# Optimization experiments

Hardware: AMD Instinct MI355X
Metric: run time of the kernel (lower is better)

## Reference

```python
import jax, jax.numpy as jnp
import numpy as np


def setup_inputs() -> dict:
    key = jax.random.key(0)
    k1, k2, k3, k4 = jax.random.split(key, 4)
    B, V, P, C, R, N, OUT = 8, 4096, 32, 32, 2, 16, 32  # N=(l_max+1)^2, l_max=3
    signal = jax.random.normal(k1, (B, V, C), dtype=jnp.float32)
    patches_idx = jax.random.randint(k2, (B, V, P), 0, V, dtype=jnp.int32)
    conv_kernel = jax.random.normal(k3, (B, V, P, R, N), dtype=jnp.float32)
    kernel_weights = jax.random.normal(k4, (OUT, C, R, N), dtype=jnp.float32) * 0.05
    biases = jnp.zeros((OUT,), dtype=jnp.float32)
    return {
        "signal": signal,
        "patches_idx": patches_idx,
        "conv_kernel": conv_kernel,
        "kernel_weights": kernel_weights,
        "biases": biases,
    }


def reference(signal, patches_idx, conv_kernel, kernel_weights, biases):
    # Gather per-vertex tree-neighbor patches (tf.gather_nd with batch idx):
    # signal [B,V,C], patches_idx [B,V,P] -> patches [B,V,P,C]
    patches = jax.vmap(lambda s, i: s[i])(signal, patches_idx)
    # Bilinear contraction with precomputed SH conv kernel: [B,V,P,R,N] x [B,V,P,C]
    y = jnp.einsum('bvprn,bvpc->bvcrn', conv_kernel, patches)
    # Learned weights contraction: [OUT,C,R,N] x [B,V,C,R,N] -> [B,V,OUT]
    y = jnp.einsum('ijrn,bvjrn->bvi', kernel_weights, y)
    y = y + biases
    return jax.nn.relu(y)
```

## Files before the change

### kernel.cpp

```cpp
#include <hip/hip_runtime.h>


typedef __attribute__((ext_vector_type(8))) short bf16x8;
typedef __attribute__((ext_vector_type(4))) short short4v;
typedef __attribute__((ext_vector_type(16))) float f32x16;
typedef __attribute__((ext_vector_type(4))) float f32x4;

__device__ __forceinline__ unsigned short f2bf_rne(float f) {
    union { float f; unsigned int u; } x;
    x.f = f;
    unsigned int u = x.u;
    return (unsigned short)((u + 0x7fffu + ((u >> 16) & 1u)) >> 16);
}
__device__ __forceinline__ unsigned short f2bf_rh(float f) {
    union { float f; unsigned int u; } x;
    x.f = f;
    return (unsigned short)((x.u + 0x8000u) >> 16);
}

__global__ __launch_bounds__(256) void prep_kernel(
        const float* __restrict__ W, const float* __restrict__ sig,
        unsigned short* __restrict__ Wf, unsigned short* __restrict__ sigbf) {
    int tid = blockIdx.x * 256 + threadIdx.x;
    if (tid < 32768) {
        int j = tid & 7;
        int l = (tid >> 3) & 63;
        int pair = tid >> 9;
        int s = pair >> 1;
        int t = pair & 1;
        int i = 16 * t + (l & 15);
        int crn = 32 * s + 8 * (l >> 4) + j;
        Wf[tid] = f2bf_rne(W[i * 1024 + crn]);
    } else {
        int e = (tid - 32768) * 8;
        if (e < 8 * 4096 * 32) {
            f32x4 a = *(const f32x4*)(sig + e);
            f32x4 b = *(const f32x4*)(sig + e + 4);
            bf16x8 v;
            v[0] = (short)f2bf_rne(a[0]); v[1] = (short)f2bf_rne(a[1]);
            v[2] = (short)f2bf_rne(a[2]); v[3] = (short)f2bf_rne(a[3]);
            v[4] = (short)f2bf_rne(b[0]); v[5] = (short)f2bf_rne(b[1]);
            v[6] = (short)f2bf_rne(b[2]); v[7] = (short)f2bf_rne(b[3]);
            *(bf16x8*)(sigbf + e) = v;
        }
    }
}

__global__ __launch_bounds__(512, 8) void fused_kernel(
        const unsigned short* __restrict__ sigbf, const int* __restrict__ pidx,
        const float* __restrict__ ck, const unsigned short* __restrict__ Wf,
        const float* __restrict__ bias, float* __restrict__ out) {
    __shared__ __align__(16) unsigned short ckb[8 * 1024];
    __shared__ __align__(16) unsigned short T_lds[8 * 1032];
    const int tid = threadIdx.x;
    const int l = tid & 63;
    const int g = l >> 5;
    const int cc = l & 31;
    const int wu = __builtin_amdgcn_readfirstlane(tid >> 6);
    const int m0 = blockIdx.x * 8;
    const int b = m0 >> 12;
    const unsigned short* sgb = sigbf + (size_t)b * (4096 * 32);

    int rows[32];
    {
        const int* ip = pidx + (size_t)(m0 + wu) * 32;
        #pragma unroll
        for (int k = 0; k < 32; ++k) rows[k] = ip[k];
    }
    f32x4 st[4];
    {
        const f32x4* ckv = (const f32x4*)(ck + (size_t)(m0 + wu) * 1024);
        #pragma unroll
        for (int i = 0; i < 4; ++i) st[i] = ckv[i * 64 + l];
    }
    unsigned short ga[16];
    #pragma unroll
    for (int h = 0; h < 2; ++h) {
        #pragma unroll
        for (int j = 0; j < 8; ++j) {
            const int rlo = rows[h * 16 + j];
            const int rhi = rows[h * 16 + 8 + j];
            const int row = g ? rhi : rlo;
            ga[h * 8 + j] = sgb[row * 32 + cc];
        }
    }
    #pragma unroll
    for (int i = 0; i < 4; ++i) {
        union { f32x4 f; unsigned int u[4]; } x;
        x.f = st[i];
        short4v v = { (short)(x.u[0] >> 16), (short)(x.u[1] >> 16),
                      (short)(x.u[2] >> 16), (short)(x.u[3] >> 16) };
        *(short4v*)(ckb + wu * 1024 + (i * 64 + l) * 4) = v;
    }
    __syncthreads();

    {
        const unsigned short* ct = ckb + wu * 1024;
        f32x16 acc = {};
        #pragma unroll
        for (int h = 0; h < 2; ++h) {
            bf16x8 af, bfr;
            #pragma unroll
            for (int j = 0; j < 8; ++j) {
                const int p = h * 16 + 8 * g + j;
                af[j]  = (short)ga[h * 8 + j];
                bfr[j] = (short)ct[p * 32 + cc];
            }
            acc = __builtin_amdgcn_mfma_f32_32x32x16_bf16(af, bfr, acc, 0, 0, 0);
        }
        unsigned short* trow = T_lds + wu * 1032 + cc + g * 128;
        #pragma unroll
        for (int r = 0; r < 16; ++r)
            trow[((r & 3) + 8 * (r >> 2)) * 32] = f2bf_rh(acc[r]);
    }
    __syncthreads();

    f32x4 acc0 = {}, acc1 = {};
    const int lg = l >> 4;
    const int ln = l & 15;
    #pragma unroll
    for (int si = 0; si < 4; ++si) {
        const int s = 4 * wu + si;
        const bf16x8 af =
            *(const bf16x8*)(T_lds + (ln & 7) * 1032 + s * 32 + 8 * lg);
        const bf16x8* wrow = (const bf16x8*)(Wf + (size_t)(s * 2) * 512);
        const bf16x8 b0 = wrow[l];
        const bf16x8 b1 = wrow[64 + l];
        acc0 = __builtin_amdgcn_mfma_f32_16x16x32_bf16(af, b0, acc0, 0, 0, 0);
        acc1 = __builtin_amdgcn_mfma_f32_16x16x32_bf16(af, b1, acc1, 0, 0, 0);
    }
    __syncthreads();

    float* red = (float*)T_lds;
    {
        f32x4* rp = (f32x4*)(red + wu * 512);
        rp[l]      = acc0;
        rp[64 + l] = acc1;
    }
    __syncthreads();

    if (tid < 256) {
        const int bv  = tid >> 5;
        const int i   = tid & 31;
        const int t   = i >> 4;
        const int col = i & 15;
        const int lgi = bv >> 2;
        const int r   = bv & 3;
        const int li  = lgi * 16 + col;
        const int o   = t * 256 + li * 4 + r;
        float sum = 0.f;
        #pragma unroll
        for (int w2 = 0; w2 < 8; ++w2) sum += red[w2 * 512 + o];
        sum += bias[i];
        out[(size_t)(m0 + bv) * 32 + i] = sum > 0.f ? sum : 0.f;
    }
}

extern "C" void kernel_launch(void* const* d_in, const int* in_sizes, int n_in,
                              void* d_out, int out_size, void* d_ws, size_t ws_size,
                              hipStream_t stream) {
    const float* sig  = (const float*)d_in[0];
    const int*   pidx = (const int*)d_in[1];
    const float* ck   = (const float*)d_in[2];
    const float* W    = (const float*)d_in[3];
    const float* bias = (const float*)d_in[4];
    float* out = (float*)d_out;
    unsigned short* Wf    = (unsigned short*)d_ws;
    unsigned short* sigbf = Wf + 32768;

    prep_kernel<<<640, 256, 0, stream>>>(W, sig, Wf, sigbf);
    fused_kernel<<<4096, 512, 0, stream>>>(sigbf, pidx, ck, Wf, bias, out);
}
```

Measured before the change: 37.00 us.

## Process two vertex groups per block with software-pipelined loads

Each block now handles 16 vertices as two groups of 8. The patch-index, conv-kernel and gather loads for the second group are issued while the first group's MFMA phases run. A second LDS buffer for the conv kernel is added, and the reduction scratch is moved into the conv-kernel buffer. The grid is halved and the occupancy hint drops from 8 to 6 to leave room for the extra registers and LDS. The aim is to hide global load latency on this bandwidth-heavy kernel, at the cost of fewer resident blocks and fewer blocks overall.

After: 39.61 us. 7.0% more time.

```diff
diff --git a/kernel.cpp b/kernel.cpp
--- a/kernel.cpp
+++ b/kernel.cpp
@@ -46,56 +46,56 @@
     }
 }
 
-__global__ __launch_bounds__(512, 8) void fused_kernel(
+__global__ __launch_bounds__(512, 6) void fused_kernel(
         const unsigned short* __restrict__ sigbf, const int* __restrict__ pidx,
         const float* __restrict__ ck, const unsigned short* __restrict__ Wf,
         const float* __restrict__ bias, float* __restrict__ out) {
-    __shared__ __align__(16) unsigned short ckb[8 * 1024];
+    __shared__ __align__(16) unsigned short ckb0[8 * 1024];
+    __shared__ __align__(16) unsigned short ckb1[8 * 1024];
     __shared__ __align__(16) unsigned short T_lds[8 * 1032];
     const int tid = threadIdx.x;
     const int l = tid & 63;
     const int g = l >> 5;
     const int cc = l & 31;
     const int wu = __builtin_amdgcn_readfirstlane(tid >> 6);
-    const int m0 = blockIdx.x * 8;
-    const int b = m0 >> 12;
+    const int mb = blockIdx.x * 16;
+    const int b = mb >> 12;
     const unsigned short* sgb = sigbf + (size_t)b * (4096 * 32);
 
-    int rows[32];
-    {
+    auto sload_rows = [&](int m0, int (&rows)[32]) {
         const int* ip = pidx + (size_t)(m0 + wu) * 32;
         #pragma unroll
         for (int k = 0; k < 32; ++k) rows[k] = ip[k];
-    }
-    f32x4 st[4];
-    {
+    };
+    auto load_st = [&](int m0, f32x4 (&st)[4]) {
         const f32x4* ckv = (const f32x4*)(ck + (size_t)(m0 + wu) * 1024);
         #pragma unroll
         for (int i = 0; i < 4; ++i) st[i] = ckv[i * 64 + l];
-    }
-    unsigned short ga[16];
-    #pragma unroll
-    for (int h = 0; h < 2; ++h) {
+    };
+    auto gather = [&](const int (&rows)[32], unsigned short (&ga)[16]) {
         #pragma unroll
-        for (int j = 0; j < 8; ++j) {
-            const int rlo = rows[h * 16 + j];
-            const int rhi = rows[h * 16 + 8 + j];
-            const int row = g ? rhi : rlo;
-            ga[h * 8 + j] = sgb[row * 32 + cc];
+        for (int h = 0; h < 2; ++h) {
+            #pragma unroll
+            for (int j = 0; j < 8; ++j) {
+                const int rlo = rows[h * 16 + j];
+                const int rhi = rows[h * 16 + 8 + j];
+                const int row = g ? rhi : rlo;
+                ga[h * 8 + j] = sgb[row * 32 + cc];
+            }
         }
-    }
-    #pragma unroll
-    for (int i = 0; i < 4; ++i) {
-        union { f32x4 f; unsigned int u[4]; } x;
-        x.f = st[i];
-        short4v v = { (short)(x.u[0] >> 16), (short)(x.u[1] >> 16),
-                      (short)(x.u[2] >> 16), (short)(x.u[3] >> 16) };
-        *(short4v*)(ckb + wu * 1024 + (i * 64 + l) * 4) = v;
-    }
-    __syncthreads();
-
-    {
-        const unsigned short* ct = ckb + wu * 1024;
+    };
+    auto pack = [&](unsigned short* buf, const f32x4 (&st)[4]) {
+        #pragma unroll
+        for (int i = 0; i < 4; ++i) {
+            union { f32x4 f; unsigned int u[4]; } x;
+            x.f = st[i];
+            short4v v = { (short)(x.u[0] >> 16), (short)(x.u[1] >> 16),
+                          (short)(x.u[2] >> 16), (short)(x.u[3] >> 16) };
+            *(short4v*)(buf + wu * 1024 + (i * 64 + l) * 4) = v;
+        }
+    };
+    auto phaseA = [&](const unsigned short* buf, const unsigned short (&ga)[16]) {
+        const unsigned short* ct = buf + wu * 1024;
         f32x16 acc = {};
         #pragma unroll
         for (int h = 0; h < 2; ++h) {
@@ -112,48 +112,69 @@
         #pragma unroll
         for (int r = 0; r < 16; ++r)
             trow[((r & 3) + 8 * (r >> 2)) * 32] = f2bf_rh(acc[r]);
-    }
-    __syncthreads();
-
-    f32x4 acc0 = {}, acc1 = {};
-    const int lg = l >> 4;
-    const int ln = l & 15;
-    #pragma unroll
-    for (int si = 0; si < 4; ++si) {
-        const int s = 4 * wu + si;
-        const bf16x8 af =
-            *(const bf16x8*)(T_lds + (ln & 7) * 1032 + s * 32 + 8 * lg);
-        const bf16x8* wrow = (const bf16x8*)(Wf + (size_t)(s * 2) * 512);
-        const bf16x8 b0 = wrow[l];
-        const bf16x8 b1 = wrow[64 + l];
-        acc0 = __builtin_amdgcn_mfma_f32_16x16x32_bf16(af, b0, acc0, 0, 0, 0);
-        acc1 = __builtin_amdgcn_mfma_f32_16x16x32_bf16(af, b1, acc1, 0, 0, 0);
-    }
-    __syncthreads();
-
-    float* red = (float*)T_lds;
-    {
-        f32x4* rp = (f32x4*)(red + wu * 512);
+    };
+    auto phaseB_red = [&](unsigned short* redbuf) {
+        f32x4 acc0 = {}, acc1 = {};
+        const int lg = l >> 4;
+        const int ln = l & 15;
+        #pragma unroll
+        for (int si = 0; si < 4; ++si) {
+            const int s = 4 * wu + si;
+            const bf16x8 af =
+                *(const bf16x8*)(T_lds + (ln & 7) * 1032 + s * 32 + 8 * lg);
+            const bf16x8* wrow = (const bf16x8*)(Wf + (size_t)(s * 2) * 512);
+            const bf16x8 b0 = wrow[l];
+            const bf16x8 b1 = wrow[64 + l];
+            acc0 = __builtin_amdgcn_mfma_f32_16x16x32_bf16(af, b0, acc0, 0, 0, 0);
+            acc1 = __builtin_amdgcn_mfma_f32_16x16x32_bf16(af, b1, acc1, 0, 0, 0);
+        }
+        f32x4* rp = (f32x4*)((float*)redbuf + wu * 512);
         rp[l]      = acc0;
         rp[64 + l] = acc1;
-    }
+    };
+    auto epilogue = [&](int m0, const unsigned short* redbuf) {
+        if (tid < 256) {
+            const float* red = (const float*)redbuf;
+            const int bv  = tid >> 5;
+            const int i   = tid & 31;
+            const int t   = i >> 4;
+            const int col = i & 15;
+            const int lgi = bv >> 2;
+            const int r   = bv & 3;
+            const int li  = lgi * 16 + col;
+            const int o   = t * 256 + li * 4 + r;
+            float sum = 0.f;
+            #pragma unroll
+            for (int w2 = 0; w2 < 8; ++w2) sum += red[w2 * 512 + o];
+            sum += bias[i];
+            out[(size_t)(m0 + bv) * 32 + i] = sum > 0.f ? sum : 0.f;
+        }
+    };
+
+    int rows0[32], rows1[32];
+    f32x4 st[4];
+    sload_rows(mb, rows0);
+    load_st(mb, st);
+    unsigned short ga0[16], ga1[16];
+    gather(rows0, ga0);
+    pack(ckb0, st);
+
+    sload_rows(mb + 8, rows1);
+    load_st(mb + 8, st);
+
+    phaseA(ckb0, ga0);
+    gather(rows1, ga1);
     __syncthreads();
+    phaseB_red(ckb0);
+    pack(ckb1, st);
+    __syncthreads();
+    epilogue(mb, ckb0);
 
-    if (tid < 256) {
-        const int bv  = tid >> 5;
-        const int i   = tid & 31;
-        const int t   = i >> 4;
-        const int col = i & 15;
-        const int lgi = bv >> 2;
-        const int r   = bv & 3;
-        const int li  = lgi * 16 + col;
-        const int o   = t * 256 + li * 4 + r;
-        float sum = 0.f;
-        #pragma unroll
-        for (int w2 = 0; w2 < 8; ++w2) sum += red[w2 * 512 + o];
-        sum += bias[i];
-        out[(size_t)(m0 + bv) * 32 + i] = sum > 0.f ? sum : 0.f;
-    }
+    phaseA(ckb1, ga1);
+    __syncthreads();
+    phaseB_red(ckb1);
+    __syncthreads();
+    epilogue(mb + 8, ckb1);
 }
 
 extern "C" void kernel_launch(void* const* d_in, const int* in_sizes, int n_in,
@@ -169,5 +190,5 @@
     unsigned short* sigbf = Wf + 32768;
 
     prep_kernel<<<640, 256, 0, stream>>>(W, sig, Wf, sigbf);
-    fused_kernel<<<4096, 512, 0, stream>>>(sigbf, pidx, ck, Wf, bias, out);
+    fused_kernel<<<2048, 512, 0, stream>>>(sigbf, pidx, ck, Wf, bias, out);
 }
```
